# Kernel optimization log

Hardware: AMD Instinct MI355X
Metric: run time of the kernel (lower is better)

The kernel has to match this reference:

```python
import jax, jax.numpy as jnp
import numpy as np

BS, M, D_IN, D_OUT = 32, 128, 64, 32


def _spd_log(X):
    # torch.svd on an SPD matrix == eigh (u diag(s) u^T with s>0), so
    # u @ diag(log s) @ v^T reduces to u @ diag(log s) @ u^T.
    s, u = jnp.linalg.eigh(X)
    return jnp.einsum('...ik,...k,...jk->...ij', u, jnp.log(s), u)


def _sym_exp(X):
    s, u = jnp.linalg.eigh(X)
    return jnp.einsum('...ik,...k,...jk->...ij', u, jnp.exp(s), u)


def setup_inputs() -> dict:
    key = jax.random.key(0)
    kx, kq, kk, kv = jax.random.split(key, 4)
    A = jax.random.normal(kx, (BS, M, D_IN, D_IN), dtype=jnp.float32)
    # SPD input: A A^T / d_in + eps I (eigenvalues strictly positive)
    x = jnp.einsum('bmij,bmkj->bmik', A, A) / D_IN + 1e-2 * jnp.eye(D_IN, dtype=jnp.float32)
    def stiefel(k):
        # column-orthonormal (d_in, d_out), mimicking SPDTransform's Stiefel weight
        return jnp.linalg.qr(jax.random.normal(k, (D_IN, D_OUT), dtype=jnp.float32))[0]
    return {'x': x, 'Wq': stiefel(kq), 'Wk': stiefel(kk), 'Wv': stiefel(kv)}


def reference(x, Wq, Wk, Wv):
    bs, m, d_in, _ = x.shape
    d_out = Wq.shape[1]

    def bimap(W):  # SPDTransform: W^T X W, stays SPD
        return jnp.einsum('pi,bmpq,qj->bmij', W, x, W)

    Q, K, V = bimap(Wq), bimap(Wk), bimap(Wv)
    logQ, logK, logV = _spd_log(Q), _spd_log(K), _spd_log(V)

    # log-Euclidean distance: sum of singular values of D D^T with
    # D = log A - log B (symmetric) equals trace(D D^T) = ||D||_F^2.
    # Torch's repeat/expand pattern yields energy[b,i,j] = d(K_i, Q_j);
    # computed here without materializing the (bs, m, m, d, d) tensor.
    q2 = jnp.sum(logQ * logQ, axis=(-2, -1))            # [bs, m]
    k2 = jnp.sum(logK * logK, axis=(-2, -1))            # [bs, m]
    cross = jnp.einsum('bikl,bjkl->bij', logK, logQ)    # [bs, m(i=K), m(j=Q)]
    energy = k2[:, :, None] + q2[:, None, :] - 2.0 * cross

    scores = 1.0 / (1.0 + jnp.log1p(energy))
    # softmax over dim=-2 (the K index i), then permute(0, 2, 1)
    attn = jnp.swapaxes(jax.nn.softmax(scores, axis=-2), -1, -2)  # [bs, j, i]

    # LogEuclideanMean: exp_sym( sum_i attn[b,j,i] * log V[b,i] )
    mean_log = jnp.einsum('bji,bikl->bjkl', attn, logV)
    out = _sym_exp(mean_log)
    return out.reshape(bs * m, d_out, d_out)
```

## Files before the change

kernel.cpp:

```cpp
#include <hip/hip_runtime.h>
#include <math.h>

constexpr int kBS = 32, kM = 128, kNMAT = kBS * kM;
constexpr int kDIN = 64, kDOUT = 32, kMSZ = kDOUT * kDOUT;
constexpr int kNSweep = 5;

constexpr size_t OFF_SS   = (size_t)3 * kNMAT * kMSZ;
constexpr size_t OFF_ATTN = OFF_SS + (size_t)3 * kNMAT;

#define F4(p)  (*(float4*)(p))
#define CF4(p) (*(const float4*)(p))

__global__ __launch_bounds__(256) void k_bimap(
    const float* __restrict__ x, const float* __restrict__ Wq,
    const float* __restrict__ Wk, const float* __restrict__ Wv,
    float* __restrict__ P) {
  __shared__ float Xs[64 * 68];
  __shared__ float Wsh[64 * 32];
  __shared__ float Ts[64 * 36];
  const int t = threadIdx.x;
  const int bm = blockIdx.x;
  const float* xp = x + (size_t)bm * (kDIN * kDIN);
  {
    const int f0 = t * 16;
    const int r = f0 >> 6, c = f0 & 63;
    const float* src = xp + f0;
    float* dst = &Xs[r * 68 + c];
#pragma unroll
    for (int i = 0; i < 4; ++i) F4(dst + 4 * i) = CF4(src + 4 * i);
  }
  const int r0 = (t >> 3) * 2;
  const int j0 = (t & 7) * 4;
  const int i2 = t >> 3;
  for (int tt = 0; tt < 3; ++tt) {
    const float* W = (tt == 0) ? Wq : ((tt == 1) ? Wk : Wv);
    __syncthreads();
    F4(&Wsh[t * 8]) = CF4(W + t * 8);
    F4(&Wsh[t * 8 + 4]) = CF4(W + t * 8 + 4);
    __syncthreads();
    float a0[4] = {0.f, 0.f, 0.f, 0.f}, a1[4] = {0.f, 0.f, 0.f, 0.f};
    for (int k = 0; k < 64; ++k) {
      const float2 x01 = *(const float2*)&Xs[k * 68 + r0];
      const float4 w = CF4(&Wsh[k * 32 + j0]);
      a0[0] += x01.x * w.x; a0[1] += x01.x * w.y; a0[2] += x01.x * w.z; a0[3] += x01.x * w.w;
      a1[0] += x01.y * w.x; a1[1] += x01.y * w.y; a1[2] += x01.y * w.z; a1[3] += x01.y * w.w;
    }
    F4(&Ts[r0 * 36 + j0])       = make_float4(a0[0], a0[1], a0[2], a0[3]);
    F4(&Ts[(r0 + 1) * 36 + j0]) = make_float4(a1[0], a1[1], a1[2], a1[3]);
    __syncthreads();
    float b4[4] = {0.f, 0.f, 0.f, 0.f};
    for (int p = 0; p < 64; ++p) {
      const float wv = Wsh[p * 32 + i2];
      const float4 tv = CF4(&Ts[p * 36 + j0]);
      b4[0] += wv * tv.x; b4[1] += wv * tv.y; b4[2] += wv * tv.z; b4[3] += wv * tv.w;
    }
    F4(&P[((size_t)tt * kNMAT + bm) * kMSZ + i2 * 32 + j0]) =
        make_float4(b4[0], b4[1], b4[2], b4[3]);
  }
}

constexpr int kJSlot = 32 * 36 + 32;
constexpr int kShl1 = 0x101, kShr1 = 0x111;

template <int CTRL>
__device__ __forceinline__ float updppf(float old_, float x) {
  return __builtin_bit_cast(float,
      __builtin_amdgcn_update_dpp(__builtin_bit_cast(int, old_),
                                  __builtin_bit_cast(int, x),
                                  CTRL, 0xf, 0xf, false));
}

__device__ __forceinline__ float xsign(float x, float s) {
  return __builtin_bit_cast(float,
      __builtin_bit_cast(int, x) ^
      (__builtin_bit_cast(int, s) & 0x80000000));
}

__global__ __launch_bounds__(256, 4) void k_jacobi_log(float* __restrict__ P,
                                                       float* __restrict__ sq) {
  __shared__ float lds[8 * kJSlot];
  const int t = threadIdx.x;
  const int wid = t >> 6, lane = t & 63;
  const int g = lane & 15;
  const int sub = (lane >> 4) & 1;
  const int off = sub * 16;
  const int mymat = lane >> 5;

  const bool is_g0 = (g == 0);
  const int p0 = is_g0 ? 31 : g;
  const int q0 = is_g0 ? 0 : 31 - g;

  for (int seq = 0; seq < 2; ++seq) {
    const size_t gbase = (size_t)blockIdx.x * 16 + wid * 4 + seq * 2;
    const size_t gid = gbase + mymat;
    float* A = P + gid * kMSZ;

    float cp[16], cq[16];
    {
      const float* pr = A + p0 * 32 + off;
      const float* qr = A + q0 * 32 + off;
#pragma unroll
      for (int i = 0; i < 16; i += 4) {
        const float4 a = CF4(pr + i);
        cp[i] = a.x; cp[i + 1] = a.y; cp[i + 2] = a.z; cp[i + 3] = a.w;
        const float4 b = CF4(qr + i);
        cq[i] = b.x; cq[i + 1] = b.y; cq[i + 2] = b.z; cq[i + 3] = b.w;
      }
    }
    float app = 0.f, aqq = 0.f;
#pragma unroll
    for (int i = 0; i < 16; ++i) {
      app = fmaf(cp[i], cp[i], app);
      aqq = fmaf(cq[i], cq[i], aqq);
    }
    app += __shfl_xor(app, 16);
    aqq += __shfl_xor(aqq, 16);

    for (int sw = 0; sw < kNSweep; ++sw) {
      for (int r = 0; r < 31; ++r) {
        float d0 = cp[0] * cq[0], d1 = cp[1] * cq[1];
#pragma unroll
        for (int i = 2; i < 16; i += 2) {
          d0 = fmaf(cp[i], cq[i], d0);
          d1 = fmaf(cp[i + 1], cq[i + 1], d1);
        }
        float apq = d0 + d1;
        apq += __shfl_xor(apq, 16);
        const float d = aqq - app;
        const float apq2 = 2.f * apq;
        float h2 = fmaf(d, d, apq2 * apq2);
        h2 = fmaxf(h2, 1e-38f);
        const float hr = __builtin_amdgcn_rsqf(h2);
        const float h = h2 * hr;
        const float den = fabsf(d) + h;
        const float t0 = apq2 * __builtin_amdgcn_rcpf(den);
        const float tt = xsign(t0, d);
        const float c = __builtin_amdgcn_rsqf(fmaf(tt, tt, 1.f));
        const float sn = tt * c;
        float np[16], nq[16];
#pragma unroll
        for (int i = 0; i < 16; ++i) {
          const float t1 = c * cp[i];
          const float t2 = sn * cp[i];
          np[i] = fmaf(-sn, cq[i], t1);
          nq[i] = fmaf(c, cq[i], t2);
        }
        const float c2 = c * c, s2 = sn * sn, cs2 = 2.f * c * sn;
        const float capp = fmaf(c2, app, fmaf(s2, aqq, -cs2 * apq));
        const float caqq = (app + aqq) - capp;
#pragma unroll
        for (int i = 0; i < 16; ++i) {
          const float cpm = updppf<kShl1>(nq[i], np[i]);
          cp[i] = is_g0 ? np[i] : cpm;
          cq[i] = updppf<kShr1>(cpm, nq[i]);
        }
        {
          const float capm = updppf<kShl1>(caqq, capp);
          app = is_g0 ? capp : capm;
          aqq = updppf<kShr1>(capm, caqq);
        }
      }
    }
    {
      float* Bs = lds + (wid * 2 + mymat) * kJSlot;
#pragma unroll
      for (int i = 0; i < 16; i += 4) {
        F4(&Bs[p0 * 36 + off + i]) = make_float4(cp[i], cp[i+1], cp[i+2], cp[i+3]);
        F4(&Bs[q0 * 36 + off + i]) = make_float4(cq[i], cq[i+1], cq[i+2], cq[i+3]);
      }
    }
    __builtin_amdgcn_wave_barrier();
#pragma unroll
    for (int m = 0; m < 2; ++m) {
      float* Bs = lds + (wid * 2 + m) * kJSlot;
      float* ncol = Bs + 1152;
      const size_t gm = gbase + m;
      float* Am = P + gm * kMSZ;
      {
        const int cc_ = lane & 31, h = lane >> 5;
        const float* col = &Bs[cc_ * 36 + h * 16];
        float ssum = 0.f;
#pragma unroll
        for (int i = 0; i < 16; i += 4) {
          const float4 v = CF4(col + i);
          ssum += v.x * v.x + v.y * v.y + v.z * v.z + v.w * v.w;
        }
        ssum += __shfl_xor(ssum, 32);
        const float lg = 0.5f * logf(ssum);
        float tot = lg * lg;
        tot += __shfl_xor(tot, 1);  tot += __shfl_xor(tot, 2);
        tot += __shfl_xor(tot, 4);  tot += __shfl_xor(tot, 8);
        tot += __shfl_xor(tot, 16); tot += __shfl_xor(tot, 32);
        if (lane == 0) sq[gm] = 0.5f * tot;
        if (h == 0) ncol[cc_] = lg / ssum;
      }
      __builtin_amdgcn_wave_barrier();
      {
        const int rr = (lane >> 3) * 4, cc = (lane & 7) * 4;
        float acc[4][4] = {};
        for (int c = 0; c < 32; ++c) {
          const float w = ncol[c];
          const float4 br = CF4(&Bs[c * 36 + rr]);
          const float4 bc = CF4(&Bs[c * 36 + cc]);
          const float wr[4]  = {w * br.x, w * br.y, w * br.z, w * br.w};
          const float bcv[4] = {bc.x, bc.y, bc.z, bc.w};
#pragma unroll
          for (int i = 0; i < 4; ++i)
#pragma unroll
            for (int j2 = 0; j2 < 4; ++j2) acc[i][j2] += wr[i] * bcv[j2];
        }
#pragma unroll
        for (int i = 0; i < 4; ++i)
          F4(&Am[(rr + i) * 32 + cc]) =
              make_float4(acc[i][0], acc[i][1], acc[i][2], acc[i][3]);
      }
      __builtin_amdgcn_wave_barrier();
    }
  }
}

__global__ __launch_bounds__(256) void k_attn(
    const float* __restrict__ P, const float* __restrict__ sq,
    float* __restrict__ attn) {
  __shared__ float Kt[32 * 132];
  __shared__ float Qt[32 * 20];
  __shared__ float Ss[128 * 20];
  __shared__ float red[16 * 20];
  __shared__ float mcol[16];
  __shared__ float scol[16];
  const int t = threadIdx.x;
  const int b = blockIdx.y, jt = blockIdx.x;
  const int j0g = jt * 16;
  const float* logK = P + ((size_t)kNMAT + (size_t)b * kM) * kMSZ;
  const float* logQ = P + ((size_t)b * kM + j0g) * kMSZ;
  const int i0 = (t >> 3) * 4, j0 = (t & 7) * 2;
  float acc[4][2] = {};
  for (int dc = 0; dc < kMSZ; dc += 32) {
    __syncthreads();
    {
      const int r = t >> 1, c0 = (t & 1) * 16;
      const float* src = logK + (size_t)r * kMSZ + dc + c0;
#pragma unroll
      for (int ii = 0; ii < 16; ii += 4) {
        const float4 v = CF4(src + ii);
        Kt[(c0 + ii + 0) * 132 + r] = v.x;
        Kt[(c0 + ii + 1) * 132 + r] = v.y;
        Kt[(c0 + ii + 2) * 132 + r] = v.z;
        Kt[(c0 + ii + 3) * 132 + r] = v.w;
      }
    }
    {
      const int j = t >> 4, c0 = (t & 15) * 2;
      const float2 v = *(const float2*)(logQ + (size_t)j * kMSZ + dc + c0);
      Qt[(c0 + 0) * 20 + j] = v.x;
      Qt[(c0 + 1) * 20 + j] = v.y;
    }
    __syncthreads();
    for (int k = 0; k < 32; ++k) {
      const float4 kv = CF4(&Kt[k * 132 + i0]);
      const float2 qv = *(const float2*)&Qt[k * 20 + j0];
      acc[0][0] = fmaf(kv.x, qv.x, acc[0][0]);
      acc[0][1] = fmaf(kv.x, qv.y, acc[0][1]);
      acc[1][0] = fmaf(kv.y, qv.x, acc[1][0]);
      acc[1][1] = fmaf(kv.y, qv.y, acc[1][1]);
      acc[2][0] = fmaf(kv.z, qv.x, acc[2][0]);
      acc[2][1] = fmaf(kv.z, qv.y, acc[2][1]);
      acc[3][0] = fmaf(kv.w, qv.x, acc[3][0]);
      acc[3][1] = fmaf(kv.w, qv.y, acc[3][1]);
    }
  }
  {
    float k2v[4], q2v[2];
#pragma unroll
    for (int i = 0; i < 4; ++i) k2v[i] = sq[kNMAT + b * kM + i0 + i];
#pragma unroll
    for (int j2 = 0; j2 < 2; ++j2) q2v[j2] = sq[b * kM + j0g + j0 + j2];
#pragma unroll
    for (int i = 0; i < 4; ++i)
#pragma unroll
      for (int j2 = 0; j2 < 2; ++j2) {
        float e = k2v[i] + q2v[j2] - 2.f * acc[i][j2];
        e = fmaxf(e, 0.f);
        Ss[(i0 + i) * 20 + (j0 + j2)] = 1.f / (1.f + log1pf(e));
      }
  }
  __syncthreads();
  const int jl = t & 15, grp = t >> 4;
  {
    float m = -1e30f;
#pragma unroll
    for (int i = 0; i < 8; ++i) m = fmaxf(m, Ss[(grp * 8 + i) * 20 + jl]);
    red[grp * 20 + jl] = m;
  }
  __syncthreads();
  if (t < 16) {
    float m = red[t];
#pragma unroll
    for (int g = 1; g < 16; ++g) m = fmaxf(m, red[g * 20 + t]);
    mcol[t] = m;
  }
  __syncthreads();
  {
    const float mj = mcol[jl];
    float s = 0.f;
#pragma unroll
    for (int i = 0; i < 8; ++i) s += expf(Ss[(grp * 8 + i) * 20 + jl] - mj);
    red[grp * 20 + jl] = s;
  }
  __syncthreads();
  if (t < 16) {
    float s = red[t];
#pragma unroll
    for (int g = 1; g < 16; ++g) s += red[g * 20 + t];
    scol[t] = 1.f / s;
  }
  __syncthreads();
  {
    const int il = t & 31, jg = t >> 5;
#pragma unroll
    for (int rep = 0; rep < 2; ++rep) {
      const int j2 = jg + rep * 8;
      const float mj = mcol[j2], is = scol[j2];
      float* dst = attn + ((size_t)b * kM + j0g + j2) * kM;
#pragma unroll
      for (int c4 = 0; c4 < 4; ++c4) {
        const int i = il + c4 * 32;
        dst[i] = expf(Ss[i * 20 + j2] - mj) * is;
      }
    }
  }
}

__global__ __launch_bounds__(256) void k_meanlog(
    const float* __restrict__ attn, const float* __restrict__ P,
    float* __restrict__ ML) {
  __shared__ float As[16 * 132];
  const int t = threadIdx.x;
  const int b = blockIdx.y, jt = blockIdx.x;
  const int j0g = jt * 16;
  const float* logV = P + ((size_t)2 * kNMAT + (size_t)b * kM) * kMSZ;
  {
    const int j = t >> 4, k0 = (t & 15) * 8;
    const float* src = attn + ((size_t)b * kM + j0g + j) * kM + k0;
    F4(&As[j * 132 + k0])     = CF4(src);
    F4(&As[j * 132 + k0 + 4]) = CF4(src + 4);
  }
  __syncthreads();
  const int d0 = t * 4;
  float acc[16][4] = {};
  for (int k = 0; k < kM; k += 4) {
    float4 vr[4];
#pragma unroll
    for (int kk = 0; kk < 4; ++kk)
      vr[kk] = CF4(&logV[(size_t)(k + kk) * kMSZ + d0]);
#pragma unroll
    for (int j = 0; j < 16; ++j) {
      const float4 w = CF4(&As[j * 132 + k]);
      const float wv[4] = {w.x, w.y, w.z, w.w};
#pragma unroll
      for (int kk = 0; kk < 4; ++kk) {
        const float* vv = (const float*)&vr[kk];
#pragma unroll
        for (int dd = 0; dd < 4; ++dd)
          acc[j][dd] = fmaf(wv[kk], vv[dd], acc[j][dd]);
      }
    }
  }
#pragma unroll
  for (int j = 0; j < 16; ++j)
    F4(&ML[((size_t)b * kM + j0g + j) * kMSZ + d0]) =
        make_float4(acc[j][0], acc[j][1], acc[j][2], acc[j][3]);
}

constexpr int kESlot = 2 * 1152;

__global__ __launch_bounds__(256) void k_expm(const float* __restrict__ ML,
                                              float* __restrict__ out) {
  __shared__ float lds[4 * kESlot];
  const int t = threadIdx.x;
  const int wid = t >> 6, lane = t & 63;
  const size_t bm = (size_t)blockIdx.x * 4 + wid;
  float* Mb = lds + wid * kESlot;
  float* Tb = Mb + 1152;
  const float* S = ML + bm * kMSZ;
  const int r = lane >> 1, c0 = (lane & 1) * 16;
  float4 v0 = CF4(S + r * 32 + c0),     v1 = CF4(S + r * 32 + c0 + 4),
         v2 = CF4(S + r * 32 + c0 + 8), v3 = CF4(S + r * 32 + c0 + 12);
  float lsum = v0.x*v0.x + v0.y*v0.y + v0.z*v0.z + v0.w*v0.w
             + v1.x*v1.x + v1.y*v1.y + v1.z*v1.z + v1.w*v1.w
             + v2.x*v2.x + v2.y*v2.y + v2.z*v2.z + v2.w*v2.w
             + v3.x*v3.x + v3.y*v3.y + v3.z*v3.z + v3.w*v3.w;
#pragma unroll
  for (int d = 1; d < 64; d <<= 1) lsum += __shfl_xor(lsum, d);
  const float fn = sqrtf(lsum);
  int sc = 0;
  if (fn > 0.5f) sc = (int)ceilf(log2f(fn * 2.0f));
  const float scale = exp2f((float)(-sc));
  v0.x*=scale; v0.y*=scale; v0.z*=scale; v0.w*=scale;
  v1.x*=scale; v1.y*=scale; v1.z*=scale; v1.w*=scale;
  v2.x*=scale; v2.y*=scale; v2.z*=scale; v2.w*=scale;
  v3.x*=scale; v3.y*=scale; v3.z*=scale; v3.w*=scale;
  F4(&Mb[r * 36 + c0])      = v0;
  F4(&Mb[r * 36 + c0 + 4])  = v1;
  F4(&Mb[r * 36 + c0 + 8])  = v2;
  F4(&Mb[r * 36 + c0 + 12]) = v3;
  __builtin_amdgcn_wave_barrier();
  const int rr = (lane >> 3) * 4, cc = (lane & 7) * 4;
#pragma unroll
  for (int i = 0; i < 4; ++i) {
    float4 v = F4(&Mb[(rr + i) * 36 + cc]);
    v.x = v.x * (1.f/7.f) + ((rr + i == cc + 0) ? 1.f : 0.f);
    v.y = v.y * (1.f/7.f) + ((rr + i == cc + 1) ? 1.f : 0.f);
    v.z = v.z * (1.f/7.f) + ((rr + i == cc + 2) ? 1.f : 0.f);
    v.w = v.w * (1.f/7.f) + ((rr + i == cc + 3) ? 1.f : 0.f);
    F4(&Tb[(rr + i) * 36 + cc]) = v;
  }
  __builtin_amdgcn_wave_barrier();
  for (int j = 6; j >= 1; --j) {
    float a4[4][4] = {};
    for (int k = 0; k < 32; ++k) {
      const float4 mv = CF4(&Mb[k * 36 + rr]);
      const float mvv[4] = {mv.x, mv.y, mv.z, mv.w};
      const float4 tv = CF4(&Tb[k * 36 + cc]);
      const float tvv[4] = {tv.x, tv.y, tv.z, tv.w};
#pragma unroll
      for (int i = 0; i < 4; ++i)
#pragma unroll
        for (int j2 = 0; j2 < 4; ++j2) a4[i][j2] += mvv[i] * tvv[j2];
    }
    const float inv = 1.f / (float)j;
#pragma unroll
    for (int i = 0; i < 4; ++i) {
      float4 v;
      v.x = a4[i][0] * inv + ((rr + i == cc + 0) ? 1.f : 0.f);
      v.y = a4[i][1] * inv + ((rr + i == cc + 1) ? 1.f : 0.f);
      v.z = a4[i][2] * inv + ((rr + i == cc + 2) ? 1.f : 0.f);
      v.w = a4[i][3] * inv + ((rr + i == cc + 3) ? 1.f : 0.f);
      F4(&Tb[(rr + i) * 36 + cc]) = v;
    }
    __builtin_amdgcn_wave_barrier();
  }
  for (int st = 0; st < sc; ++st) {
    float a4[4][4] = {};
    for (int k = 0; k < 32; ++k) {
      const float4 mv = CF4(&Tb[k * 36 + rr]);
      const float mvv[4] = {mv.x, mv.y, mv.z, mv.w};
      const float4 tv = CF4(&Tb[k * 36 + cc]);
      const float tvv[4] = {tv.x, tv.y, tv.z, tv.w};
#pragma unroll
      for (int i = 0; i < 4; ++i)
#pragma unroll
        for (int j2 = 0; j2 < 4; ++j2) a4[i][j2] += mvv[i] * tvv[j2];
    }
#pragma unroll
    for (int i = 0; i < 4; ++i)
      F4(&Tb[(rr + i) * 36 + cc]) =
          make_float4(a4[i][0], a4[i][1], a4[i][2], a4[i][3]);
    __builtin_amdgcn_wave_barrier();
  }
#pragma unroll
  for (int i = 0; i < 4; ++i) {
    const float4 v = CF4(&Tb[(rr + i) * 36 + cc]);
    F4(&out[bm * kMSZ + (rr + i) * 32 + cc]) = v;
  }
}

extern "C" void kernel_launch(void* const* d_in, const int* in_sizes, int n_in,
                              void* d_out, int out_size, void* d_ws, size_t ws_size,
                              hipStream_t stream) {
  const float* x  = (const float*)d_in[0];
  const float* Wq = (const float*)d_in[1];
  const float* Wk = (const float*)d_in[2];
  const float* Wv = (const float*)d_in[3];
  float* ws   = (float*)d_ws;
  float* P    = ws;
  float* sq   = ws + OFF_SS;
  float* attn = ws + OFF_ATTN;
  float* ML   = ws;
  float* out  = (float*)d_out;

  k_bimap<<<kNMAT, 256, 0, stream>>>(x, Wq, Wk, Wv, P);
  k_jacobi_log<<<3 * kNMAT / 16, 256, 0, stream>>>(P, sq);
  k_attn<<<dim3(8, kBS), 256, 0, stream>>>(P, sq, attn);
  k_meanlog<<<dim3(8, kBS), 256, 0, stream>>>(attn, P, ML);
  k_expm<<<kNMAT / 4, 256, 0, stream>>>(ML, out);
}
```

Measured before the change: 468.6 us.

## Process four matrices per wave with full 32-wide columns per lane in Jacobi

Restructures the one-sided Jacobi eigen kernel so each 16-lane group owns a whole matrix and each lane holds two full 32-element columns, instead of splitting columns across two 16-lane halves. This removes the cross-half shuffle reductions in every rotation step and the sequential two-pass loop, since four matrices now run concurrently per wave. Column norms and log weights are computed in registers before staging to LDS one matrix at a time for reconstruction. The cost is double the register footprint per lane (64 column floats), which may reduce occupancy under the launch bound of 4 blocks per CU.

New measurement: 588.5 us. 25.6% more time.

```diff
diff --git a/kernel.cpp b/kernel.cpp
--- a/kernel.cpp
+++ b/kernel.cpp
@@ -78,144 +78,139 @@
 
 __global__ __launch_bounds__(256, 4) void k_jacobi_log(float* __restrict__ P,
                                                        float* __restrict__ sq) {
-  __shared__ float lds[8 * kJSlot];
+  __shared__ float lds[4 * kJSlot];
   const int t = threadIdx.x;
   const int wid = t >> 6, lane = t & 63;
   const int g = lane & 15;
-  const int sub = (lane >> 4) & 1;
-  const int off = sub * 16;
-  const int mymat = lane >> 5;
+  const int grp = lane >> 4;
 
   const bool is_g0 = (g == 0);
   const int p0 = is_g0 ? 31 : g;
   const int q0 = is_g0 ? 0 : 31 - g;
 
-  for (int seq = 0; seq < 2; ++seq) {
-    const size_t gbase = (size_t)blockIdx.x * 16 + wid * 4 + seq * 2;
-    const size_t gid = gbase + mymat;
-    float* A = P + gid * kMSZ;
-
-    float cp[16], cq[16];
+  const size_t gbase = (size_t)blockIdx.x * 16 + wid * 4;
+  const float* A = P + (gbase + grp) * kMSZ;
+
+  float cp[32], cq[32];
+  {
+    const float* pr = A + p0 * 32;
+    const float* qr = A + q0 * 32;
+#pragma unroll
+    for (int i = 0; i < 32; i += 4) {
+      const float4 a = CF4(pr + i);
+      cp[i] = a.x; cp[i + 1] = a.y; cp[i + 2] = a.z; cp[i + 3] = a.w;
+      const float4 b = CF4(qr + i);
+      cq[i] = b.x; cq[i + 1] = b.y; cq[i + 2] = b.z; cq[i + 3] = b.w;
+    }
+  }
+  float app, aqq;
+  {
+    float p0a = cp[0]*cp[0], p1a = cp[1]*cp[1];
+    float q0a = cq[0]*cq[0], q1a = cq[1]*cq[1];
+#pragma unroll
+    for (int i = 2; i < 32; i += 2) {
+      p0a = fmaf(cp[i], cp[i], p0a);  p1a = fmaf(cp[i+1], cp[i+1], p1a);
+      q0a = fmaf(cq[i], cq[i], q0a);  q1a = fmaf(cq[i+1], cq[i+1], q1a);
+    }
+    app = p0a + p1a;
+    aqq = q0a + q1a;
+  }
+
+  for (int sw = 0; sw < kNSweep; ++sw) {
+    for (int r = 0; r < 31; ++r) {
+      float d0 = cp[0]*cq[0], d1 = cp[1]*cq[1], d2 = cp[2]*cq[2], d3 = cp[3]*cq[3];
+#pragma unroll
+      for (int i = 4; i < 32; i += 4) {
+        d0 = fmaf(cp[i],     cq[i],     d0);
+        d1 = fmaf(cp[i + 1], cq[i + 1], d1);
+        d2 = fmaf(cp[i + 2], cq[i + 2], d2);
+        d3 = fmaf(cp[i + 3], cq[i + 3], d3);
+      }
+      const float apq = (d0 + d1) + (d2 + d3);
+      const float d = aqq - app;
+      const float apq2 = 2.f * apq;
+      float h2 = fmaf(d, d, apq2 * apq2);
+      h2 = fmaxf(h2, 1e-38f);
+      const float hr = __builtin_amdgcn_rsqf(h2);
+      const float h = h2 * hr;
+      const float den = fabsf(d) + h;
+      const float t0 = apq2 * __builtin_amdgcn_rcpf(den);
+      const float tt = xsign(t0, d);
+      const float c = __builtin_amdgcn_rsqf(fmaf(tt, tt, 1.f));
+      const float sn = tt * c;
+#pragma unroll
+      for (int i = 0; i < 32; ++i) {
+        const float np = fmaf(-sn, cq[i], c * cp[i]);
+        const float nq = fmaf(c, cq[i], sn * cp[i]);
+        const float cpm = updppf<kShl1>(nq, np);
+        cp[i] = is_g0 ? np : cpm;
+        cq[i] = updppf<kShr1>(cpm, nq);
+      }
+      const float c2 = c * c, s2 = sn * sn, cs2 = 2.f * c * sn;
+      const float capp = fmaf(c2, app, fmaf(s2, aqq, -cs2 * apq));
+      const float caqq = (app + aqq) - capp;
+      const float capm = updppf<kShl1>(caqq, capp);
+      app = is_g0 ? capp : capm;
+      aqq = updppf<kShr1>(capm, caqq);
+    }
+  }
+  float ssp, ssq;
+  {
+    float p0a = cp[0]*cp[0], p1a = cp[1]*cp[1];
+    float q0a = cq[0]*cq[0], q1a = cq[1]*cq[1];
+#pragma unroll
+    for (int i = 2; i < 32; i += 2) {
+      p0a = fmaf(cp[i], cp[i], p0a);  p1a = fmaf(cp[i+1], cp[i+1], p1a);
+      q0a = fmaf(cq[i], cq[i], q0a);  q1a = fmaf(cq[i+1], cq[i+1], q1a);
+    }
+    ssp = p0a + p1a;
+    ssq = q0a + q1a;
+  }
+  const float lgp = 0.5f * logf(ssp);
+  const float lgq = 0.5f * logf(ssq);
+  const float wp = lgp * __builtin_amdgcn_rcpf(ssp);
+  const float wq = lgq * __builtin_amdgcn_rcpf(ssq);
+  {
+    float tot = fmaf(lgp, lgp, lgq * lgq);
+    tot += __shfl_xor(tot, 1); tot += __shfl_xor(tot, 2);
+    tot += __shfl_xor(tot, 4); tot += __shfl_xor(tot, 8);
+    if (g == 0) sq[gbase + grp] = tot;
+  }
+  float* Bs = lds + wid * kJSlot;
+  float* ncol = Bs + 1152;
+  for (int m = 0; m < 4; ++m) {
+    __builtin_amdgcn_wave_barrier();
+    if (grp == m) {
+#pragma unroll
+      for (int i = 0; i < 32; i += 4) {
+        F4(&Bs[p0 * 36 + i]) = make_float4(cp[i], cp[i+1], cp[i+2], cp[i+3]);
+        F4(&Bs[q0 * 36 + i]) = make_float4(cq[i], cq[i+1], cq[i+2], cq[i+3]);
+      }
+      ncol[p0] = wp;
+      ncol[q0] = wq;
+    }
+    __builtin_amdgcn_wave_barrier();
     {
-      const float* pr = A + p0 * 32 + off;
-      const float* qr = A + q0 * 32 + off;
-#pragma unroll
-      for (int i = 0; i < 16; i += 4) {
-        const float4 a = CF4(pr + i);
-        cp[i] = a.x; cp[i + 1] = a.y; cp[i + 2] = a.z; cp[i + 3] = a.w;
-        const float4 b = CF4(qr + i);
-        cq[i] = b.x; cq[i + 1] = b.y; cq[i + 2] = b.z; cq[i + 3] = b.w;
-      }
-    }
-    float app = 0.f, aqq = 0.f;
-#pragma unroll
-    for (int i = 0; i < 16; ++i) {
-      app = fmaf(cp[i], cp[i], app);
-      aqq = fmaf(cq[i], cq[i], aqq);
-    }
-    app += __shfl_xor(app, 16);
-    aqq += __shfl_xor(aqq, 16);
-
-    for (int sw = 0; sw < kNSweep; ++sw) {
-      for (int r = 0; r < 31; ++r) {
-        float d0 = cp[0] * cq[0], d1 = cp[1] * cq[1];
-#pragma unroll
-        for (int i = 2; i < 16; i += 2) {
-          d0 = fmaf(cp[i], cq[i], d0);
-          d1 = fmaf(cp[i + 1], cq[i + 1], d1);
-        }
-        float apq = d0 + d1;
-        apq += __shfl_xor(apq, 16);
-        const float d = aqq - app;
-        const float apq2 = 2.f * apq;
-        float h2 = fmaf(d, d, apq2 * apq2);
-        h2 = fmaxf(h2, 1e-38f);
-        const float hr = __builtin_amdgcn_rsqf(h2);
-        const float h = h2 * hr;
-        const float den = fabsf(d) + h;
-        const float t0 = apq2 * __builtin_amdgcn_rcpf(den);
-        const float tt = xsign(t0, d);
-        const float c = __builtin_amdgcn_rsqf(fmaf(tt, tt, 1.f));
-        const float sn = tt * c;
-        float np[16], nq[16];
-#pragma unroll
-        for (int i = 0; i < 16; ++i) {
-          const float t1 = c * cp[i];
-          const float t2 = sn * cp[i];
-          np[i] = fmaf(-sn, cq[i], t1);
-          nq[i] = fmaf(c, cq[i], t2);
-        }
-        const float c2 = c * c, s2 = sn * sn, cs2 = 2.f * c * sn;
-        const float capp = fmaf(c2, app, fmaf(s2, aqq, -cs2 * apq));
-        const float caqq = (app + aqq) - capp;
-#pragma unroll
-        for (int i = 0; i < 16; ++i) {
-          const float cpm = updppf<kShl1>(nq[i], np[i]);
-          cp[i] = is_g0 ? np[i] : cpm;
-          cq[i] = updppf<kShr1>(cpm, nq[i]);
-        }
-        {
-          const float capm = updppf<kShl1>(caqq, capp);
-          app = is_g0 ? capp : capm;
-          aqq = updppf<kShr1>(capm, caqq);
-        }
-      }
-    }
-    {
-      float* Bs = lds + (wid * 2 + mymat) * kJSlot;
-#pragma unroll
-      for (int i = 0; i < 16; i += 4) {
-        F4(&Bs[p0 * 36 + off + i]) = make_float4(cp[i], cp[i+1], cp[i+2], cp[i+3]);
-        F4(&Bs[q0 * 36 + off + i]) = make_float4(cq[i], cq[i+1], cq[i+2], cq[i+3]);
-      }
+      float* Am = P + (gbase + m) * kMSZ;
+      const int rr = (lane >> 3) * 4, cc = (lane & 7) * 4;
+      float acc[4][4] = {};
+      for (int c = 0; c < 32; ++c) {
+        const float w = ncol[c];
+        const float4 br = CF4(&Bs[c * 36 + rr]);
+        const float4 bc = CF4(&Bs[c * 36 + cc]);
+        const float wr[4]  = {w * br.x, w * br.y, w * br.z, w * br.w};
+        const float bcv[4] = {bc.x, bc.y, bc.z, bc.w};
+#pragma unroll
+        for (int i = 0; i < 4; ++i)
+#pragma unroll
+          for (int j2 = 0; j2 < 4; ++j2) acc[i][j2] += wr[i] * bcv[j2];
+      }
+#pragma unroll
+      for (int i = 0; i < 4; ++i)
+        F4(&Am[(rr + i) * 32 + cc]) =
+            make_float4(acc[i][0], acc[i][1], acc[i][2], acc[i][3]);
     }
     __builtin_amdgcn_wave_barrier();
-#pragma unroll
-    for (int m = 0; m < 2; ++m) {
-      float* Bs = lds + (wid * 2 + m) * kJSlot;
-      float* ncol = Bs + 1152;
-      const size_t gm = gbase + m;
-      float* Am = P + gm * kMSZ;
-      {
-        const int cc_ = lane & 31, h = lane >> 5;
-        const float* col = &Bs[cc_ * 36 + h * 16];
-        float ssum = 0.f;
-#pragma unroll
-        for (int i = 0; i < 16; i += 4) {
-          const float4 v = CF4(col + i);
-          ssum += v.x * v.x + v.y * v.y + v.z * v.z + v.w * v.w;
-        }
-        ssum += __shfl_xor(ssum, 32);
-        const float lg = 0.5f * logf(ssum);
-        float tot = lg * lg;
-        tot += __shfl_xor(tot, 1);  tot += __shfl_xor(tot, 2);
-        tot += __shfl_xor(tot, 4);  tot += __shfl_xor(tot, 8);
-        tot += __shfl_xor(tot, 16); tot += __shfl_xor(tot, 32);
-        if (lane == 0) sq[gm] = 0.5f * tot;
-        if (h == 0) ncol[cc_] = lg / ssum;
-      }
-      __builtin_amdgcn_wave_barrier();
-      {
-        const int rr = (lane >> 3) * 4, cc = (lane & 7) * 4;
-        float acc[4][4] = {};
-        for (int c = 0; c < 32; ++c) {
-          const float w = ncol[c];
-          const float4 br = CF4(&Bs[c * 36 + rr]);
-          const float4 bc = CF4(&Bs[c * 36 + cc]);
-          const float wr[4]  = {w * br.x, w * br.y, w * br.z, w * br.w};
-          const float bcv[4] = {bc.x, bc.y, bc.z, bc.w};
-#pragma unroll
-          for (int i = 0; i < 4; ++i)
-#pragma unroll
-            for (int j2 = 0; j2 < 4; ++j2) acc[i][j2] += wr[i] * bcv[j2];
-        }
-#pragma unroll
-        for (int i = 0; i < 4; ++i)
-          F4(&Am[(rr + i) * 32 + cc]) =
-              make_float4(acc[i][0], acc[i][1], acc[i][2], acc[i][3]);
-      }
-      __builtin_amdgcn_wave_barrier();
-    }
   }
 }
 
```

## Process one matrix pair per wave and compute eigen-log weights in registers

Applied to the files above, without the earlier changes.

The Jacobi-log kernel drops its sequential two-pass loop, so each wave handles one pair of matrices and twice as many blocks are launched. The LDS footprint is halved because a single slot per wave is reused for both matrices in turn. Column norms, log weights and the squared-log sum are now computed directly from register-resident columns instead of re-reading LDS. This is meant to expose more parallelism and shorten the reconstruction tail, at the cost of more blocks and serialized LDS reuse between the two matrices.

Result: faster. 458.5 us (-2.2%).

```diff
diff --git a/kernel.cpp b/kernel.cpp
--- a/kernel.cpp
+++ b/kernel.cpp
@@ -78,144 +78,142 @@
 
 __global__ __launch_bounds__(256, 4) void k_jacobi_log(float* __restrict__ P,
                                                        float* __restrict__ sq) {
-  __shared__ float lds[8 * kJSlot];
+  __shared__ float lds[4 * kJSlot];
   const int t = threadIdx.x;
   const int wid = t >> 6, lane = t & 63;
+  const int mat = lane >> 5;
   const int g = lane & 15;
   const int sub = (lane >> 4) & 1;
   const int off = sub * 16;
-  const int mymat = lane >> 5;
 
   const bool is_g0 = (g == 0);
   const int p0 = is_g0 ? 31 : g;
   const int q0 = is_g0 ? 0 : 31 - g;
 
-  for (int seq = 0; seq < 2; ++seq) {
-    const size_t gbase = (size_t)blockIdx.x * 16 + wid * 4 + seq * 2;
-    const size_t gid = gbase + mymat;
-    float* A = P + gid * kMSZ;
-
-    float cp[16], cq[16];
-    {
-      const float* pr = A + p0 * 32 + off;
-      const float* qr = A + q0 * 32 + off;
-#pragma unroll
-      for (int i = 0; i < 16; i += 4) {
-        const float4 a = CF4(pr + i);
-        cp[i] = a.x; cp[i + 1] = a.y; cp[i + 2] = a.z; cp[i + 3] = a.w;
-        const float4 b = CF4(qr + i);
-        cq[i] = b.x; cq[i + 1] = b.y; cq[i + 2] = b.z; cq[i + 3] = b.w;
-      }
-    }
-    float app = 0.f, aqq = 0.f;
-#pragma unroll
-    for (int i = 0; i < 16; ++i) {
-      app = fmaf(cp[i], cp[i], app);
-      aqq = fmaf(cq[i], cq[i], aqq);
-    }
-    app += __shfl_xor(app, 16);
-    aqq += __shfl_xor(aqq, 16);
-
-    for (int sw = 0; sw < kNSweep; ++sw) {
-      for (int r = 0; r < 31; ++r) {
-        float d0 = cp[0] * cq[0], d1 = cp[1] * cq[1];
-#pragma unroll
-        for (int i = 2; i < 16; i += 2) {
-          d0 = fmaf(cp[i], cq[i], d0);
-          d1 = fmaf(cp[i + 1], cq[i + 1], d1);
-        }
-        float apq = d0 + d1;
-        apq += __shfl_xor(apq, 16);
-        const float d = aqq - app;
-        const float apq2 = 2.f * apq;
-        float h2 = fmaf(d, d, apq2 * apq2);
-        h2 = fmaxf(h2, 1e-38f);
-        const float hr = __builtin_amdgcn_rsqf(h2);
-        const float h = h2 * hr;
-        const float den = fabsf(d) + h;
-        const float t0 = apq2 * __builtin_amdgcn_rcpf(den);
-        const float tt = xsign(t0, d);
-        const float c = __builtin_amdgcn_rsqf(fmaf(tt, tt, 1.f));
-        const float sn = tt * c;
-        float np[16], nq[16];
-#pragma unroll
-        for (int i = 0; i < 16; ++i) {
-          const float t1 = c * cp[i];
-          const float t2 = sn * cp[i];
-          np[i] = fmaf(-sn, cq[i], t1);
-          nq[i] = fmaf(c, cq[i], t2);
-        }
-        const float c2 = c * c, s2 = sn * sn, cs2 = 2.f * c * sn;
-        const float capp = fmaf(c2, app, fmaf(s2, aqq, -cs2 * apq));
-        const float caqq = (app + aqq) - capp;
-#pragma unroll
-        for (int i = 0; i < 16; ++i) {
-          const float cpm = updppf<kShl1>(nq[i], np[i]);
-          cp[i] = is_g0 ? np[i] : cpm;
-          cq[i] = updppf<kShr1>(cpm, nq[i]);
-        }
-        {
-          const float capm = updppf<kShl1>(caqq, capp);
-          app = is_g0 ? capp : capm;
-          aqq = updppf<kShr1>(capm, caqq);
-        }
-      }
-    }
-    {
-      float* Bs = lds + (wid * 2 + mymat) * kJSlot;
+  const size_t gbase = (size_t)blockIdx.x * 8 + wid * 2;
+  const float* A = P + (gbase + mat) * kMSZ;
+
+  float cp[16], cq[16];
+  {
+    const float* pr = A + p0 * 32 + off;
+    const float* qr = A + q0 * 32 + off;
+#pragma unroll
+    for (int i = 0; i < 16; i += 4) {
+      const float4 a = CF4(pr + i);
+      cp[i] = a.x; cp[i + 1] = a.y; cp[i + 2] = a.z; cp[i + 3] = a.w;
+      const float4 b = CF4(qr + i);
+      cq[i] = b.x; cq[i + 1] = b.y; cq[i + 2] = b.z; cq[i + 3] = b.w;
+    }
+  }
+  float app = 0.f, aqq = 0.f;
+#pragma unroll
+  for (int i = 0; i < 16; ++i) {
+    app = fmaf(cp[i], cp[i], app);
+    aqq = fmaf(cq[i], cq[i], aqq);
+  }
+  app += __shfl_xor(app, 16);
+  aqq += __shfl_xor(aqq, 16);
+
+  for (int sw = 0; sw < kNSweep; ++sw) {
+    for (int r = 0; r < 31; ++r) {
+      float d0 = cp[0] * cq[0], d1 = cp[1] * cq[1];
+#pragma unroll
+      for (int i = 2; i < 16; i += 2) {
+        d0 = fmaf(cp[i], cq[i], d0);
+        d1 = fmaf(cp[i + 1], cq[i + 1], d1);
+      }
+      float apq = d0 + d1;
+      apq += __shfl_xor(apq, 16);
+      const float d = aqq - app;
+      const float apq2 = 2.f * apq;
+      float h2 = fmaf(d, d, apq2 * apq2);
+      h2 = fmaxf(h2, 1e-38f);
+      const float hr = __builtin_amdgcn_rsqf(h2);
+      const float h = h2 * hr;
+      const float den = fabsf(d) + h;
+      const float t0 = apq2 * __builtin_amdgcn_rcpf(den);
+      const float tt = xsign(t0, d);
+      const float c = __builtin_amdgcn_rsqf(fmaf(tt, tt, 1.f));
+      const float sn = tt * c;
+      float np[16], nq[16];
+#pragma unroll
+      for (int i = 0; i < 16; ++i) {
+        const float t1 = c * cp[i];
+        const float t2 = sn * cp[i];
+        np[i] = fmaf(-sn, cq[i], t1);
+        nq[i] = fmaf(c, cq[i], t2);
+      }
+      const float c2 = c * c, s2 = sn * sn, cs2 = 2.f * c * sn;
+      const float capp = fmaf(c2, app, fmaf(s2, aqq, -cs2 * apq));
+      const float caqq = (app + aqq) - capp;
+#pragma unroll
+      for (int i = 0; i < 16; ++i) {
+        const float cpm = updppf<kShl1>(nq[i], np[i]);
+        cp[i] = is_g0 ? np[i] : cpm;
+        cq[i] = updppf<kShr1>(cpm, nq[i]);
+      }
+      {
+        const float capm = updppf<kShl1>(caqq, capp);
+        app = is_g0 ? capp : capm;
+        aqq = updppf<kShr1>(capm, caqq);
+      }
+    }
+  }
+  float ssp = 0.f, ssq = 0.f;
+#pragma unroll
+  for (int i = 0; i < 16; ++i) {
+    ssp = fmaf(cp[i], cp[i], ssp);
+    ssq = fmaf(cq[i], cq[i], ssq);
+  }
+  ssp += __shfl_xor(ssp, 16);
+  ssq += __shfl_xor(ssq, 16);
+  const float lgp = 0.5f * logf(ssp);
+  const float lgq = 0.5f * logf(ssq);
+  const float wp = lgp * __builtin_amdgcn_rcpf(ssp);
+  const float wq = lgq * __builtin_amdgcn_rcpf(ssq);
+  {
+    float tot = fmaf(lgp, lgp, lgq * lgq);
+    tot += __shfl_xor(tot, 1); tot += __shfl_xor(tot, 2);
+    tot += __shfl_xor(tot, 4); tot += __shfl_xor(tot, 8);
+    if ((lane & 31) == 0) sq[gbase + mat] = tot;
+  }
+  float* Bs = lds + wid * kJSlot;
+  float* ncol = Bs + 1152;
+  for (int m = 0; m < 2; ++m) {
+    __builtin_amdgcn_wave_barrier();
+    if (mat == m) {
 #pragma unroll
       for (int i = 0; i < 16; i += 4) {
         F4(&Bs[p0 * 36 + off + i]) = make_float4(cp[i], cp[i+1], cp[i+2], cp[i+3]);
         F4(&Bs[q0 * 36 + off + i]) = make_float4(cq[i], cq[i+1], cq[i+2], cq[i+3]);
       }
+      if (sub == 0) {
+        ncol[p0] = wp;
+        ncol[q0] = wq;
+      }
     }
     __builtin_amdgcn_wave_barrier();
-#pragma unroll
-    for (int m = 0; m < 2; ++m) {
-      float* Bs = lds + (wid * 2 + m) * kJSlot;
-      float* ncol = Bs + 1152;
-      const size_t gm = gbase + m;
-      float* Am = P + gm * kMSZ;
-      {
-        const int cc_ = lane & 31, h = lane >> 5;
-        const float* col = &Bs[cc_ * 36 + h * 16];
-        float ssum = 0.f;
-#pragma unroll
-        for (int i = 0; i < 16; i += 4) {
-          const float4 v = CF4(col + i);
-          ssum += v.x * v.x + v.y * v.y + v.z * v.z + v.w * v.w;
-        }
-        ssum += __shfl_xor(ssum, 32);
-        const float lg = 0.5f * logf(ssum);
-        float tot = lg * lg;
-        tot += __shfl_xor(tot, 1);  tot += __shfl_xor(tot, 2);
-        tot += __shfl_xor(tot, 4);  tot += __shfl_xor(tot, 8);
-        tot += __shfl_xor(tot, 16); tot += __shfl_xor(tot, 32);
-        if (lane == 0) sq[gm] = 0.5f * tot;
-        if (h == 0) ncol[cc_] = lg / ssum;
-      }
-      __builtin_amdgcn_wave_barrier();
-      {
-        const int rr = (lane >> 3) * 4, cc = (lane & 7) * 4;
-        float acc[4][4] = {};
-        for (int c = 0; c < 32; ++c) {
-          const float w = ncol[c];
-          const float4 br = CF4(&Bs[c * 36 + rr]);
-          const float4 bc = CF4(&Bs[c * 36 + cc]);
-          const float wr[4]  = {w * br.x, w * br.y, w * br.z, w * br.w};
-          const float bcv[4] = {bc.x, bc.y, bc.z, bc.w};
-#pragma unroll
-          for (int i = 0; i < 4; ++i)
-#pragma unroll
-            for (int j2 = 0; j2 < 4; ++j2) acc[i][j2] += wr[i] * bcv[j2];
-        }
+    {
+      float* Am = P + (gbase + m) * kMSZ;
+      const int rr = (lane >> 3) * 4, cc = (lane & 7) * 4;
+      float acc[4][4] = {};
+      for (int c = 0; c < 32; ++c) {
+        const float w = ncol[c];
+        const float4 br = CF4(&Bs[c * 36 + rr]);
+        const float4 bc = CF4(&Bs[c * 36 + cc]);
+        const float wr[4]  = {w * br.x, w * br.y, w * br.z, w * br.w};
+        const float bcv[4] = {bc.x, bc.y, bc.z, bc.w};
 #pragma unroll
         for (int i = 0; i < 4; ++i)
-          F4(&Am[(rr + i) * 32 + cc]) =
-              make_float4(acc[i][0], acc[i][1], acc[i][2], acc[i][3]);
-      }
-      __builtin_amdgcn_wave_barrier();
-    }
+#pragma unroll
+          for (int j2 = 0; j2 < 4; ++j2) acc[i][j2] += wr[i] * bcv[j2];
+      }
+#pragma unroll
+      for (int i = 0; i < 4; ++i)
+        F4(&Am[(rr + i) * 32 + cc]) =
+            make_float4(acc[i][0], acc[i][1], acc[i][2], acc[i][3]);
+    }
+    __builtin_amdgcn_wave_barrier();
   }
 }
 
@@ -480,7 +478,7 @@
   float* out  = (float*)d_out;
 
   k_bimap<<<kNMAT, 256, 0, stream>>>(x, Wq, Wk, Wv, P);
-  k_jacobi_log<<<3 * kNMAT / 16, 256, 0, stream>>>(P, sq);
+  k_jacobi_log<<<3 * kNMAT / 8, 256, 0, stream>>>(P, sq);
   k_attn<<<dim3(8, kBS), 256, 0, stream>>>(P, sq, attn);
   k_meanlog<<<dim3(8, kBS), 256, 0, stream>>>(attn, P, ML);
   k_expm<<<kNMAT / 4, 256, 0, stream>>>(ML, out);
```
